# Kernel optimization log

Measured on AMD Instinct MI355X. Metric: run time of the kernel, lower is better.

The kernel has to match this reference:

```python
import jax, jax.numpy as jnp
import numpy as np

P, N, NF = 4, 871, 512            # num_meta_paths, node_size (hardcoded 871 in source), node_feature_size
XDIM = 116 * 116                   # x_proj input dim, hardcoded Linear(116*116, nf)
BETA, LAMBDA_WL, GAMMA = 0.1, 0.1, 0.1


def _xavier(k, shape):
    fan_in, fan_out = shape[0], shape[-1]
    bound = np.sqrt(6.0 / (fan_in + fan_out))
    return jax.random.uniform(k, shape, jnp.float32, -bound, bound)


def setup_inputs() -> dict:
    key = jax.random.key(0)
    ks = jax.random.split(key, 12)
    return {
        "z_stack": jax.random.normal(ks[0], (P, N, NF), jnp.float32),
        "x_orig": jax.random.normal(ks[1], (1, 116, 116), jnp.float32),
        "W": _xavier(ks[2], (N, 1)),
        "b": jax.random.uniform(ks[3], (N, 1), jnp.float32),
        "q": _xavier(ks[4], (N, NF)),
        "xp_w": _xavier(ks[5], (XDIM, NF)),
        "xp_b": jnp.zeros((NF,), jnp.float32),
        "w1": _xavier(ks[6], (2 * NF, 512)), "b1": jnp.zeros((512,), jnp.float32),
        "w2": _xavier(ks[7], (512, 256)), "b2": jnp.zeros((256,), jnp.float32),
        "w3": _xavier(ks[8], (256, 1)), "b3": jnp.zeros((1,), jnp.float32),
        "perm": jax.random.permutation(ks[9], N).astype(jnp.int32),
    }


def _mi_mlp(t, w1, b1, w2, b2, w3, b3):
    h = jax.nn.relu(t @ w1 + b1)
    h = jax.nn.relu(h @ w2 + b2)
    return h @ w3 + b3  # [N, 1]


def reference(z_stack, x_orig, W, b, q, xp_w, xp_b, w1, b1, w2, b2, w3, b3, perm):
    # --- vectorized form of the per-node loop:
    # score_p = mean_i( tanh(W_i * z[p,i,:] + b_i) . q_i )
    zt = jnp.tanh(W[None] * z_stack + b[None])            # [P,N,NF]
    scores = jnp.mean(jnp.sum(zt * q[None], axis=-1), axis=-1)  # [P]
    proportions = scores / jnp.sum(scores)
    attn = jax.nn.softmax(proportions)                    # [P] (no isomorphic pairs -> no overwrite)
    # layer_out_p = attn_p * z_p + z_p ; emb = sum_p layer_out_p
    emb = jnp.einsum('p,pnf->nf', 1.0 + attn, z_stack)    # [N,NF]
    # --- estimate_MI(x_orig, emb, mi_estimator_xz)
    x = jnp.broadcast_to(x_orig.reshape(1, -1), (N, XDIM))
    xh = x @ xp_w + xp_b                                  # [N,NF]
    t0 = jnp.concatenate([xh, emb], axis=1)               # [N,2NF]
    t1 = jnp.concatenate([xh, emb[perm]], axis=1)
    mi_lb = jnp.mean(_mi_mlp(t0, w1, b1, w2, b2, w3, b3)) - jnp.log(
        jnp.mean(jnp.exp(_mi_mlp(t1, w1, b1, w2, b2, w3, b3))) + 1e-8)
    I_XZ = jnp.clip(mi_lb, 0.0)
    # y_labels=None -> I_ZY = 0 ; empty isomorphic_pairs -> wl_loss = 0
    total_loss = I_XZ - BETA * 0.0 + LAMBDA_WL * 0.0 + GAMMA * jnp.sum(attn)
    return emb, total_loss
```

## Files before the change

### kernel.cpp

```cpp
#include <hip/hip_runtime.h>
#include <hip/hip_bf16.h>
#include <math.h>

#define NMETA  4
#define NNODE  871
#define NFEAT  512
#define XDIM   (116*116)
#define ZPLANE (NNODE*NFEAT)
#define MT     55

#define NXB    175
#define XROWS  77

#define WS_SPART  16
#define WS_C1P    256
#define WS_XHP    8448
#define WS_V      98304
#define WS_W1P    99328
#define WS_W2P    230400
#define WS_FXHP   263168
#define WS_FPACK  263344
#define WS_FC1    263368
#define WS_FSP    263376
#define WS_FV     263436
#define MAGICF    0x13579BDFu

typedef short v8s __attribute__((ext_vector_type(8)));
typedef float v4f __attribute__((ext_vector_type(4)));

static __device__ __forceinline__ short f2bf(float f) {
  __hip_bfloat16 h = __float2bfloat16(f);
  return *reinterpret_cast<short*>(&h);
}

static __device__ __forceinline__ unsigned ldflag(const float* ws, int off) {
  return __hip_atomic_load((const unsigned*)&ws[off], __ATOMIC_RELAXED,
                           __HIP_MEMORY_SCOPE_AGENT);
}
static __device__ __forceinline__ void stflag(float* ws, int off) {
  __builtin_amdgcn_fence(__ATOMIC_RELEASE, "agent");
  __hip_atomic_store((unsigned*)&ws[off], MAGICF, __ATOMIC_RELAXED,
                     __HIP_MEMORY_SCOPE_AGENT);
}

__global__ __launch_bounds__(1024) void k_all(const float* __restrict__ z,
                                              const float* __restrict__ x,
                                              const float* __restrict__ W,
                                              const float* __restrict__ b,
                                              const float* __restrict__ q,
                                              const float* __restrict__ xpw,
                                              const float* __restrict__ xpb,
                                              const float* __restrict__ w1,
                                              const float* __restrict__ b1,
                                              const float* __restrict__ w2,
                                              const float* __restrict__ b2,
                                              const float* __restrict__ w3,
                                              const float* __restrict__ b3,
                                              float* __restrict__ ws,
                                              float* __restrict__ out,
                                              short* __restrict__ w1p,
                                              short* __restrict__ w2p) {
  __shared__ __align__(16) char pool[37376];
  const int blk = blockIdx.x;
  const int tid = threadIdx.x;

  if (blk < MT) {
    short* embs = (short*)pool;
    short* h2a  = (short*)(pool + 16384);
    float* cs   = (float*)(pool + 32768);
    float* spl  = (float*)(pool + 34816);
    float* sred = (float*)(pool + 35712);
    float* cf   = (float*)(pool + 35968);
    float* vred = (float*)(pool + 36000);
    float* wred = (float*)(pool + 37088);

    const int r0 = blk * 16;
    const int oc = tid & 63;
    const int row = tid >> 6;
    const int gr = r0 + row;
    const bool valid = gr < NNODE;

    const float4* z4 = (const float4*)z;
    const float4* q4 = (const float4*)q;
    float4 za0, za1, zb0, zb1, zc0, zc1, zd0, zd1, qa, qb;
    float wi = 0.f, bi = 0.f;
    const int zi = gr * 128 + oc * 2;
    if (valid) {
      za0 = z4[zi];                 za1 = z4[zi + 1];
      zb0 = z4[NNODE*128 + zi];     zb1 = z4[NNODE*128 + zi + 1];
      zc0 = z4[2*NNODE*128 + zi];   zc1 = z4[2*NNODE*128 + zi + 1];
      zd0 = z4[3*NNODE*128 + zi];   zd1 = z4[3*NNODE*128 + zi + 1];
      qa  = q4[gr * 128 + oc * 2];  qb  = q4[gr * 128 + oc * 2 + 1];
      wi = W[gr]; bi = b[gr];
    } else {
      za0 = za1 = zb0 = zb1 = zc0 = zc1 = zd0 = zd1 = (float4){0,0,0,0};
      qa = qb = (float4){0,0,0,0};
    }

    auto dot8 = [&](const float4& u0, const float4& u1) -> float {
      return tanhf(wi*u0.x + bi)*qa.x + tanhf(wi*u0.y + bi)*qa.y
           + tanhf(wi*u0.z + bi)*qa.z + tanhf(wi*u0.w + bi)*qa.w
           + tanhf(wi*u1.x + bi)*qb.x + tanhf(wi*u1.y + bi)*qb.y
           + tanhf(wi*u1.z + bi)*qb.z + tanhf(wi*u1.w + bi)*qb.w;
    };
    float sp0 = valid ? dot8(za0, za1) : 0.f;
    float sp1 = valid ? dot8(zb0, zb1) : 0.f;
    float sp2 = valid ? dot8(zc0, zc1) : 0.f;
    float sp3 = valid ? dot8(zd0, zd1) : 0.f;
#pragma unroll
    for (int m = 1; m < 64; m <<= 1) {
      sp0 += __shfl_xor(sp0, m); sp1 += __shfl_xor(sp1, m);
      sp2 += __shfl_xor(sp2, m); sp3 += __shfl_xor(sp3, m);
    }
    if (oc == 0) {
      sred[row*4+0] = sp0; sred[row*4+1] = sp1;
      sred[row*4+2] = sp2; sred[row*4+3] = sp3;
    }
    __syncthreads();
    if (tid < 4) {
      float s = 0.f;
#pragma unroll
      for (int r = 0; r < 16; ++r) s += sred[r*4 + tid];
      ws[WS_SPART + tid * 55 + blk] = s;
    }
    __syncthreads();
    if (tid == 0) stflag(ws, WS_FSP + blk);

    for (;;) {
      int ok = 1;
      if (tid < 55) ok = (ldflag(ws, WS_FSP + tid) == MAGICF);
      if (__syncthreads_and(ok)) break;
      __builtin_amdgcn_s_sleep(2);
    }
    __builtin_amdgcn_fence(__ATOMIC_ACQUIRE, "agent");
    if (tid < 220) spl[tid] = ws[WS_SPART + tid];
    __syncthreads();
    if (tid == 0) {
      float sv[NMETA], sum = 0.f;
#pragma unroll
      for (int p = 0; p < NMETA; ++p) {
        float s = 0.f;
        for (int c = 0; c < MT; ++c) s += spl[p * 55 + c];
        sv[p] = s / (float)NNODE;
        sum += sv[p];
      }
      float m = -1e30f;
#pragma unroll
      for (int p = 0; p < NMETA; ++p) { sv[p] = sv[p] / sum; m = fmaxf(m, sv[p]); }
      float es = 0.f;
#pragma unroll
      for (int p = 0; p < NMETA; ++p) { sv[p] = expf(sv[p] - m); es += sv[p]; }
#pragma unroll
      for (int p = 0; p < NMETA; ++p) cf[p] = 1.f + sv[p] / es;
    }
    __syncthreads();
    const float c0 = cf[0], c1c = cf[1], c2 = cf[2], c3 = cf[3];

    {
      const int slot = oc * 16 + (row ^ (oc & 15));
      v8s h;
      if (valid) {
        float4 r0v, r1v;
        r0v.x = c0*za0.x + c1c*zb0.x + c2*zc0.x + c3*zd0.x;
        r0v.y = c0*za0.y + c1c*zb0.y + c2*zc0.y + c3*zd0.y;
        r0v.z = c0*za0.z + c1c*zb0.z + c2*zc0.z + c3*zd0.z;
        r0v.w = c0*za0.w + c1c*zb0.w + c2*zc0.w + c3*zd0.w;
        r1v.x = c0*za1.x + c1c*zb1.x + c2*zc1.x + c3*zd1.x;
        r1v.y = c0*za1.y + c1c*zb1.y + c2*zc1.y + c3*zd1.y;
        r1v.z = c0*za1.z + c1c*zb1.z + c2*zc1.z + c3*zd1.z;
        r1v.w = c0*za1.w + c1c*zb1.w + c2*zc1.w + c3*zd1.w;
        ((float4*)out)[zi] = r0v;
        ((float4*)out)[zi + 1] = r1v;
        h[0] = f2bf(r0v.x); h[1] = f2bf(r0v.y); h[2] = f2bf(r0v.z); h[3] = f2bf(r0v.w);
        h[4] = f2bf(r1v.x); h[5] = f2bf(r1v.y); h[6] = f2bf(r1v.z); h[7] = f2bf(r1v.w);
      } else {
        h = (v8s){0,0,0,0,0,0,0,0};
      }
      *(v8s*)(embs + slot * 8) = h;
    }
    __syncthreads();

    for (;;) {
      int ok = 1;
      if (tid < 16) ok = (ldflag(ws, WS_FPACK + tid) == MAGICF);
      else if (tid < 20) ok = (ldflag(ws, WS_FC1 + (tid - 16)) == MAGICF);
      if (__syncthreads_and(ok)) break;
      __builtin_amdgcn_s_sleep(2);
    }
    __builtin_amdgcn_fence(__ATOMIC_ACQUIRE, "agent");
    if (tid < 512) {
      float a = 0.f;
#pragma unroll
      for (int k = 0; k < 4; ++k) a += ws[WS_C1P + k * 512 + tid];
      cs[tid] = a;
    }
    __syncthreads();

    const int lane = tid & 63, w = tid >> 6;
    const int n15 = lane & 15, quad = lane >> 4;
    v4f e[2];
#pragma unroll
    for (int ct = 0; ct < 2; ++ct) e[ct] = (v4f){0.f, 0.f, 0.f, 0.f};
#pragma unroll
    for (int kb = 0; kb < 16; ++kb) {
      const int koct = kb * 4 + quad;
      v8s a = *(const v8s*)(embs + (koct * 16 + (n15 ^ (koct & 15))) * 8);
      const short* B = w1p + kb * 16384 + w * 1024 + quad * 128 + n15 * 8;
#pragma unroll
      for (int ct = 0; ct < 2; ++ct) {
        v8s bb = *(const v8s*)(B + ct * 512);
        e[ct] = __builtin_amdgcn_mfma_f32_16x16x32_bf16(a, bb, e[ct], 0, 0, 0);
      }
    }
#pragma unroll
    for (int ct = 0; ct < 2; ++ct) {
      const int col = w * 32 + ct * 16 + n15;
      const int koct = col >> 3, j = col & 7;
#pragma unroll
      for (int r = 0; r < 4; ++r) {
        const int m = quad * 4 + r;
        h2a[(koct * 16 + (m ^ (koct & 15))) * 8 + j] = f2bf(fmaxf(e[ct][r] + cs[col], 0.f));
      }
    }
    __syncthreads();

    for (;;) {
      int ok = 1;
      if (tid < 4) ok = (ldflag(ws, WS_FPACK + 16 + tid) == MAGICF);
      if (__syncthreads_and(ok)) break;
      __builtin_amdgcn_s_sleep(2);
    }
    __builtin_amdgcn_fence(__ATOMIC_ACQUIRE, "agent");

    v4f g = (v4f){0.f, 0.f, 0.f, 0.f};
#pragma unroll
    for (int kb = 0; kb < 16; ++kb) {
      const int koct = kb * 4 + quad;
      v8s a = *(const v8s*)(h2a + (koct * 16 + (n15 ^ (koct & 15))) * 8);
      v8s bb = *(const v8s*)(w2p + kb * 8192 + w * 512 + quad * 128 + n15 * 8);
      g = __builtin_amdgcn_mfma_f32_16x16x32_bf16(a, bb, g, 0, 0, 0);
    }
    {
      const int col = w * 16 + n15;
      const float b2v = b2[col], w3v = w3[col];
#pragma unroll
      for (int r = 0; r < 4; ++r) {
        float s = fmaxf(g[r] + b2v, 0.f) * w3v;
        s += __shfl_xor(s, 1);
        s += __shfl_xor(s, 2);
        s += __shfl_xor(s, 4);
        s += __shfl_xor(s, 8);
        if (n15 == 0) vred[(quad * 4 + r) * 17 + w] = s;
      }
    }
    __syncthreads();
    if (tid < 16) {
      float acc = 0.f;
#pragma unroll
      for (int ww = 0; ww < 16; ++ww) acc += vred[tid * 17 + ww];
      const int grow = r0 + tid;
      if (grow < NNODE) ws[WS_V + grow] = acc;
    }
    __syncthreads();
    if (tid == 0) stflag(ws, WS_FV + blk);

    if (blk == 0) {
      for (;;) {
        int ok = 1;
        if (tid < 55) ok = (ldflag(ws, WS_FV + tid) == MAGICF);
        if (__syncthreads_and(ok)) break;
        __builtin_amdgcn_s_sleep(2);
      }
      __builtin_amdgcn_fence(__ATOMIC_ACQUIRE, "agent");
      const float bias = b3[0];
      float s0 = 0.f, s1 = 0.f;
      if (tid < NNODE) {
        float xv = ws[WS_V + tid] + bias;
        s0 = xv; s1 = expf(xv);
      }
#pragma unroll
      for (int m = 1; m < 64; m <<= 1) { s0 += __shfl_xor(s0, m); s1 += __shfl_xor(s1, m); }
      if (lane == 0) { wred[w * 2] = s0; wred[w * 2 + 1] = s1; }
      __syncthreads();
      if (tid == 0) {
        float t0 = 0.f, t1 = 0.f;
#pragma unroll
        for (int ww = 0; ww < 16; ++ww) { t0 += wred[ww * 2]; t1 += wred[ww * 2 + 1]; }
        float m0 = t0 / (float)NNODE;
        float m1 = t1 / (float)NNODE;
        float mi = m0 - logf(m1 + 1e-8f);
        out[ZPLANE] = fmaxf(mi, 0.f) + 0.1f;
      }
    }
  } else if (blk < MT + NXB) {
    const int xb = blk - MT;
    const int d0 = xb * XROWS;
    const int rows = min(XROWS, XDIM - d0);
    float* xs = (float*)pool;
    float4* redx = (float4*)(pool + 320);
    if (tid < rows) xs[tid] = x[d0 + tid];
    __syncthreads();
    const int f4 = tid & 127;
    const int rp = tid >> 7;
    float4 acc = {0.f, 0.f, 0.f, 0.f};
    const float4* xp4 = (const float4*)xpw;
    for (int r = rp; r < rows; r += 8) {
      const float xv = xs[r];
      const float4 wv = xp4[(size_t)(d0 + r) * 128 + f4];
      acc.x += xv * wv.x; acc.y += xv * wv.y; acc.z += xv * wv.z; acc.w += xv * wv.w;
    }
    if (rp) redx[(rp - 1) * 128 + f4] = acc;
    __syncthreads();
    if (!rp) {
#pragma unroll
      for (int g = 0; g < 7; ++g) {
        float4 t = redx[g * 128 + f4];
        acc.x += t.x; acc.y += t.y; acc.z += t.z; acc.w += t.w;
      }
      ((float4*)(ws + WS_XHP + (size_t)xb * 512))[f4] = acc;
    }
    __syncthreads();
    if (tid == 0) stflag(ws, WS_FXHP + xb);
  } else if (blk < MT + NXB + 4) {
    const int bk = blk - (MT + NXB);
    float* xh = (float*)pool;
    float* redr = (float*)(pool + 512);
    float4* redg = (float4*)(pool + 4608);
    for (;;) {
      int ok = 1;
      if (tid < NXB) ok = (ldflag(ws, WS_FXHP + tid) == MAGICF);
      if (__syncthreads_and(ok)) break;
      __builtin_amdgcn_s_sleep(2);
    }
    __builtin_amdgcn_fence(__ATOMIC_ACQUIRE, "agent");
    const int f = tid & 127;
    const int part = tid >> 7;
    {
      float s = 0.f;
      for (int p = part; p < NXB; p += 8) s += ws[WS_XHP + (size_t)p * 512 + bk * 128 + f];
      redr[tid] = s;
    }
    __syncthreads();
    if (tid < 128) {
      float t = xpb[bk * 128 + tid];
#pragma unroll
      for (int g = 0; g < 8; ++g) t += redr[g * 128 + tid];
      xh[tid] = t;
    }
    __syncthreads();
    const int j4 = tid & 127;
    const int fg = tid >> 7;
    float4 acc = {0.f, 0.f, 0.f, 0.f};
    const float4* w14 = (const float4*)w1;
#pragma unroll
    for (int ff = 0; ff < 16; ++ff) {
      const int fr = bk * 128 + fg * 16 + ff;
      const float xv = xh[fg * 16 + ff];
      const float4 wv = w14[(size_t)fr * 128 + j4];
      acc.x += xv * wv.x; acc.y += xv * wv.y; acc.z += xv * wv.z; acc.w += xv * wv.w;
    }
    if (fg) redg[(fg - 1) * 128 + j4] = acc;
    __syncthreads();
    if (!fg) {
#pragma unroll
      for (int g = 0; g < 7; ++g) {
        float4 t = redg[g * 128 + j4];
        acc.x += t.x; acc.y += t.y; acc.z += t.z; acc.w += t.w;
      }
      if (bk == 0) {
        acc.x += b1[j4 * 4 + 0]; acc.y += b1[j4 * 4 + 1];
        acc.z += b1[j4 * 4 + 2]; acc.w += b1[j4 * 4 + 3];
      }
      ((float4*)(ws + WS_C1P + (size_t)bk * 512))[j4] = acc;
    }
    __syncthreads();
    if (tid == 0) stflag(ws, WS_FC1 + bk);
  } else {
    const int pb = blk - (MT + NXB + 4);
    if (pb < 16) {
      const int s0 = pb * 16384;
#pragma unroll
      for (int it = 0; it < 16; ++it) {
        const int s = s0 + it * 1024 + tid;
        const int k = s >> 9, n = s & 511;
        const int t = (k >> 5) * 16384 + (n >> 4) * 512 + ((k >> 3) & 3) * 128
                    + (n & 15) * 8 + (k & 7);
        w1p[t] = f2bf(w1[(size_t)(512 + k) * 512 + n]);
      }
    } else {
      const int o0 = (pb - 16) * 16384;
#pragma unroll
      for (int it = 0; it < 16; ++it) {
        const int o = o0 + it * 1024 + tid;
        const int k = o >> 8, n = o & 255;
        const int t = (k >> 5) * 8192 + (n >> 4) * 512 + ((k >> 3) & 3) * 128
                    + (n & 15) * 8 + (k & 7);
        w2p[t] = f2bf(w2[(size_t)k * 256 + n]);
      }
    }
    __syncthreads();
    if (tid == 0) stflag(ws, WS_FPACK + pb);
  }
}

extern "C" void kernel_launch(void* const* d_in, const int* in_sizes, int n_in,
                              void* d_out, int out_size, void* d_ws, size_t ws_size,
                              hipStream_t stream) {
  const float* z   = (const float*)d_in[0];
  const float* x   = (const float*)d_in[1];
  const float* W   = (const float*)d_in[2];
  const float* b   = (const float*)d_in[3];
  const float* q   = (const float*)d_in[4];
  const float* xpw = (const float*)d_in[5];
  const float* xpb = (const float*)d_in[6];
  const float* w1  = (const float*)d_in[7];
  const float* b1  = (const float*)d_in[8];
  const float* w2  = (const float*)d_in[9];
  const float* b2  = (const float*)d_in[10];
  const float* w3  = (const float*)d_in[11];
  const float* b3  = (const float*)d_in[12];
  float* out = (float*)d_out;
  float* ws  = (float*)d_ws;

  short* w1p = (short*)(ws + WS_W1P);
  short* w2p = (short*)(ws + WS_W2P);

  k_all<<<MT + NXB + 4 + 20, 1024, 0, stream>>>(z, x, W, b, q, xpw, xpb, w1, b1,
                                                w2, b2, w3, b3, ws, out, w1p, w2p);
}
```

Baseline: 152.1 us.

## Split persistent kernel into front and fused kernels, replacing spin-wait flags

Splits the single flag-synchronized kernel into two launches. The first launch computes the x-projection partials, the score partials, the weight packing and the first-layer constant. The second launch computes emb and runs both MLP layers, then finishes with a last-block atomic-counter reduction for the MI term. Most inter-block spin-waits are replaced by the kernel boundary, and the x-projection is spread over more blocks with fewer rows each. The cost is one extra launch. The z tile is also read twice (once per kernel), and the c1 blocks still spin on x-projection flags inside the first kernel.

Measured after the change: 143.8 us. 1.06x faster.

```diff
diff --git a/kernel.cpp b/kernel.cpp
--- a/kernel.cpp
+++ b/kernel.cpp
@@ -9,20 +9,17 @@
 #define ZPLANE (NNODE*NFEAT)
 #define MT     55
 
-#define NXB    175
-#define XROWS  77
-
+#define NXB    254
+#define XROWS  53
+
+#define WS_CNT    12
 #define WS_SPART  16
 #define WS_C1P    256
-#define WS_XHP    8448
-#define WS_V      98304
-#define WS_W1P    99328
-#define WS_W2P    230400
-#define WS_FXHP   263168
-#define WS_FPACK  263344
-#define WS_FC1    263368
-#define WS_FSP    263376
-#define WS_FV     263436
+#define WS_XHP    2560
+#define WS_V      132608
+#define WS_W1P    133504
+#define WS_W2P    264576
+#define WS_FXHP   297344
 #define MAGICF    0x13579BDFu
 
 typedef short v8s __attribute__((ext_vector_type(8)));
@@ -43,60 +40,71 @@
                      __HIP_MEMORY_SCOPE_AGENT);
 }
 
-__global__ __launch_bounds__(1024) void k_all(const float* __restrict__ z,
-                                              const float* __restrict__ x,
-                                              const float* __restrict__ W,
-                                              const float* __restrict__ b,
-                                              const float* __restrict__ q,
-                                              const float* __restrict__ xpw,
-                                              const float* __restrict__ xpb,
-                                              const float* __restrict__ w1,
-                                              const float* __restrict__ b1,
-                                              const float* __restrict__ w2,
-                                              const float* __restrict__ b2,
-                                              const float* __restrict__ w3,
-                                              const float* __restrict__ b3,
-                                              float* __restrict__ ws,
-                                              float* __restrict__ out,
-                                              short* __restrict__ w1p,
-                                              short* __restrict__ w2p) {
-  __shared__ __align__(16) char pool[37376];
+__global__ __launch_bounds__(1024) void k_front(const float* __restrict__ x,
+                                                const float* __restrict__ xpw,
+                                                const float* __restrict__ w1,
+                                                const float* __restrict__ w2,
+                                                const float* __restrict__ z,
+                                                const float* __restrict__ W,
+                                                const float* __restrict__ b,
+                                                const float* __restrict__ q,
+                                                const float* __restrict__ xpb,
+                                                const float* __restrict__ b1,
+                                                float* __restrict__ ws,
+                                                short* __restrict__ w1p,
+                                                short* __restrict__ w2p) {
   const int blk = blockIdx.x;
   const int tid = threadIdx.x;
 
-  if (blk < MT) {
-    short* embs = (short*)pool;
-    short* h2a  = (short*)(pool + 16384);
-    float* cs   = (float*)(pool + 32768);
-    float* spl  = (float*)(pool + 34816);
-    float* sred = (float*)(pool + 35712);
-    float* cf   = (float*)(pool + 35968);
-    float* vred = (float*)(pool + 36000);
-    float* wred = (float*)(pool + 37088);
-
-    const int r0 = blk * 16;
+  if (blk < NXB) {
+    const int d0 = blk * XROWS;
+    const int rows = min(XROWS, XDIM - d0);
+    __shared__ float xs[XROWS];
+    __shared__ float4 redx[7][128];
+    if (tid < rows) xs[tid] = x[d0 + tid];
+    __syncthreads();
+    const int f4 = tid & 127;
+    const int g = tid >> 7;
+    float4 acc = {0.f, 0.f, 0.f, 0.f};
+    const float4* xp4 = (const float4*)xpw;
+    for (int r = g; r < rows; r += 8) {
+      const float xv = xs[r];
+      const float4 wv = xp4[(size_t)(d0 + r) * 128 + f4];
+      acc.x += xv * wv.x; acc.y += xv * wv.y; acc.z += xv * wv.z; acc.w += xv * wv.w;
+    }
+    if (g) redx[g - 1][f4] = acc;
+    __syncthreads();
+    if (!g) {
+#pragma unroll
+      for (int k = 0; k < 7; ++k) {
+        float4 t = redx[k][f4];
+        acc.x += t.x; acc.y += t.y; acc.z += t.z; acc.w += t.w;
+      }
+      ((float4*)(ws + WS_XHP + (size_t)blk * 512))[f4] = acc;
+    }
+    __syncthreads();
+    if (tid == 0) stflag(ws, WS_FXHP + blk);
+  } else if (blk < NXB + MT) {
+    const int sb = blk - NXB;
+    const int row = tid >> 6;
     const int oc = tid & 63;
-    const int row = tid >> 6;
-    const int gr = r0 + row;
+    const int gr = sb * 16 + row;
     const bool valid = gr < NNODE;
-
     const float4* z4 = (const float4*)z;
     const float4* q4 = (const float4*)q;
     float4 za0, za1, zb0, zb1, zc0, zc1, zd0, zd1, qa, qb;
     float wi = 0.f, bi = 0.f;
+    za0 = za1 = zb0 = zb1 = zc0 = zc1 = zd0 = zd1 = (float4){0,0,0,0};
+    qa = qb = (float4){0,0,0,0};
     const int zi = gr * 128 + oc * 2;
     if (valid) {
       za0 = z4[zi];                 za1 = z4[zi + 1];
       zb0 = z4[NNODE*128 + zi];     zb1 = z4[NNODE*128 + zi + 1];
       zc0 = z4[2*NNODE*128 + zi];   zc1 = z4[2*NNODE*128 + zi + 1];
       zd0 = z4[3*NNODE*128 + zi];   zd1 = z4[3*NNODE*128 + zi + 1];
-      qa  = q4[gr * 128 + oc * 2];  qb  = q4[gr * 128 + oc * 2 + 1];
+      qa  = q4[zi];                 qb  = q4[zi + 1];
       wi = W[gr]; bi = b[gr];
-    } else {
-      za0 = za1 = zb0 = zb1 = zc0 = zc1 = zd0 = zd1 = (float4){0,0,0,0};
-      qa = qb = (float4){0,0,0,0};
-    }
-
+    }
     auto dot8 = [&](const float4& u0, const float4& u1) -> float {
       return tanhf(wi*u0.x + bi)*qa.x + tanhf(wi*u0.y + bi)*qa.y
            + tanhf(wi*u0.z + bi)*qa.z + tanhf(wi*u0.w + bi)*qa.w
@@ -112,271 +120,20 @@
       sp0 += __shfl_xor(sp0, m); sp1 += __shfl_xor(sp1, m);
       sp2 += __shfl_xor(sp2, m); sp3 += __shfl_xor(sp3, m);
     }
+    __shared__ float sred[16][4];
     if (oc == 0) {
-      sred[row*4+0] = sp0; sred[row*4+1] = sp1;
-      sred[row*4+2] = sp2; sred[row*4+3] = sp3;
+      sred[row][0] = sp0; sred[row][1] = sp1;
+      sred[row][2] = sp2; sred[row][3] = sp3;
     }
     __syncthreads();
     if (tid < 4) {
       float s = 0.f;
 #pragma unroll
-      for (int r = 0; r < 16; ++r) s += sred[r*4 + tid];
-      ws[WS_SPART + tid * 55 + blk] = s;
-    }
-    __syncthreads();
-    if (tid == 0) stflag(ws, WS_FSP + blk);
-
-    for (;;) {
-      int ok = 1;
-      if (tid < 55) ok = (ldflag(ws, WS_FSP + tid) == MAGICF);
-      if (__syncthreads_and(ok)) break;
-      __builtin_amdgcn_s_sleep(2);
-    }
-    __builtin_amdgcn_fence(__ATOMIC_ACQUIRE, "agent");
-    if (tid < 220) spl[tid] = ws[WS_SPART + tid];
-    __syncthreads();
-    if (tid == 0) {
-      float sv[NMETA], sum = 0.f;
-#pragma unroll
-      for (int p = 0; p < NMETA; ++p) {
-        float s = 0.f;
-        for (int c = 0; c < MT; ++c) s += spl[p * 55 + c];
-        sv[p] = s / (float)NNODE;
-        sum += sv[p];
-      }
-      float m = -1e30f;
-#pragma unroll
-      for (int p = 0; p < NMETA; ++p) { sv[p] = sv[p] / sum; m = fmaxf(m, sv[p]); }
-      float es = 0.f;
-#pragma unroll
-      for (int p = 0; p < NMETA; ++p) { sv[p] = expf(sv[p] - m); es += sv[p]; }
-#pragma unroll
-      for (int p = 0; p < NMETA; ++p) cf[p] = 1.f + sv[p] / es;
-    }
-    __syncthreads();
-    const float c0 = cf[0], c1c = cf[1], c2 = cf[2], c3 = cf[3];
-
-    {
-      const int slot = oc * 16 + (row ^ (oc & 15));
-      v8s h;
-      if (valid) {
-        float4 r0v, r1v;
-        r0v.x = c0*za0.x + c1c*zb0.x + c2*zc0.x + c3*zd0.x;
-        r0v.y = c0*za0.y + c1c*zb0.y + c2*zc0.y + c3*zd0.y;
-        r0v.z = c0*za0.z + c1c*zb0.z + c2*zc0.z + c3*zd0.z;
-        r0v.w = c0*za0.w + c1c*zb0.w + c2*zc0.w + c3*zd0.w;
-        r1v.x = c0*za1.x + c1c*zb1.x + c2*zc1.x + c3*zd1.x;
-        r1v.y = c0*za1.y + c1c*zb1.y + c2*zc1.y + c3*zd1.y;
-        r1v.z = c0*za1.z + c1c*zb1.z + c2*zc1.z + c3*zd1.z;
-        r1v.w = c0*za1.w + c1c*zb1.w + c2*zc1.w + c3*zd1.w;
-        ((float4*)out)[zi] = r0v;
-        ((float4*)out)[zi + 1] = r1v;
-        h[0] = f2bf(r0v.x); h[1] = f2bf(r0v.y); h[2] = f2bf(r0v.z); h[3] = f2bf(r0v.w);
-        h[4] = f2bf(r1v.x); h[5] = f2bf(r1v.y); h[6] = f2bf(r1v.z); h[7] = f2bf(r1v.w);
-      } else {
-        h = (v8s){0,0,0,0,0,0,0,0};
-      }
-      *(v8s*)(embs + slot * 8) = h;
-    }
-    __syncthreads();
-
-    for (;;) {
-      int ok = 1;
-      if (tid < 16) ok = (ldflag(ws, WS_FPACK + tid) == MAGICF);
-      else if (tid < 20) ok = (ldflag(ws, WS_FC1 + (tid - 16)) == MAGICF);
-      if (__syncthreads_and(ok)) break;
-      __builtin_amdgcn_s_sleep(2);
-    }
-    __builtin_amdgcn_fence(__ATOMIC_ACQUIRE, "agent");
-    if (tid < 512) {
-      float a = 0.f;
-#pragma unroll
-      for (int k = 0; k < 4; ++k) a += ws[WS_C1P + k * 512 + tid];
-      cs[tid] = a;
-    }
-    __syncthreads();
-
-    const int lane = tid & 63, w = tid >> 6;
-    const int n15 = lane & 15, quad = lane >> 4;
-    v4f e[2];
-#pragma unroll
-    for (int ct = 0; ct < 2; ++ct) e[ct] = (v4f){0.f, 0.f, 0.f, 0.f};
-#pragma unroll
-    for (int kb = 0; kb < 16; ++kb) {
-      const int koct = kb * 4 + quad;
-      v8s a = *(const v8s*)(embs + (koct * 16 + (n15 ^ (koct & 15))) * 8);
-      const short* B = w1p + kb * 16384 + w * 1024 + quad * 128 + n15 * 8;
-#pragma unroll
-      for (int ct = 0; ct < 2; ++ct) {
-        v8s bb = *(const v8s*)(B + ct * 512);
-        e[ct] = __builtin_amdgcn_mfma_f32_16x16x32_bf16(a, bb, e[ct], 0, 0, 0);
-      }
-    }
-#pragma unroll
-    for (int ct = 0; ct < 2; ++ct) {
-      const int col = w * 32 + ct * 16 + n15;
-      const int koct = col >> 3, j = col & 7;
-#pragma unroll
-      for (int r = 0; r < 4; ++r) {
-        const int m = quad * 4 + r;
-        h2a[(koct * 16 + (m ^ (koct & 15))) * 8 + j] = f2bf(fmaxf(e[ct][r] + cs[col], 0.f));
-      }
-    }
-    __syncthreads();
-
-    for (;;) {
-      int ok = 1;
-      if (tid < 4) ok = (ldflag(ws, WS_FPACK + 16 + tid) == MAGICF);
-      if (__syncthreads_and(ok)) break;
-      __builtin_amdgcn_s_sleep(2);
-    }
-    __builtin_amdgcn_fence(__ATOMIC_ACQUIRE, "agent");
-
-    v4f g = (v4f){0.f, 0.f, 0.f, 0.f};
-#pragma unroll
-    for (int kb = 0; kb < 16; ++kb) {
-      const int koct = kb * 4 + quad;
-      v8s a = *(const v8s*)(h2a + (koct * 16 + (n15 ^ (koct & 15))) * 8);
-      v8s bb = *(const v8s*)(w2p + kb * 8192 + w * 512 + quad * 128 + n15 * 8);
-      g = __builtin_amdgcn_mfma_f32_16x16x32_bf16(a, bb, g, 0, 0, 0);
-    }
-    {
-      const int col = w * 16 + n15;
-      const float b2v = b2[col], w3v = w3[col];
-#pragma unroll
-      for (int r = 0; r < 4; ++r) {
-        float s = fmaxf(g[r] + b2v, 0.f) * w3v;
-        s += __shfl_xor(s, 1);
-        s += __shfl_xor(s, 2);
-        s += __shfl_xor(s, 4);
-        s += __shfl_xor(s, 8);
-        if (n15 == 0) vred[(quad * 4 + r) * 17 + w] = s;
-      }
-    }
-    __syncthreads();
-    if (tid < 16) {
-      float acc = 0.f;
-#pragma unroll
-      for (int ww = 0; ww < 16; ++ww) acc += vred[tid * 17 + ww];
-      const int grow = r0 + tid;
-      if (grow < NNODE) ws[WS_V + grow] = acc;
-    }
-    __syncthreads();
-    if (tid == 0) stflag(ws, WS_FV + blk);
-
-    if (blk == 0) {
-      for (;;) {
-        int ok = 1;
-        if (tid < 55) ok = (ldflag(ws, WS_FV + tid) == MAGICF);
-        if (__syncthreads_and(ok)) break;
-        __builtin_amdgcn_s_sleep(2);
-      }
-      __builtin_amdgcn_fence(__ATOMIC_ACQUIRE, "agent");
-      const float bias = b3[0];
-      float s0 = 0.f, s1 = 0.f;
-      if (tid < NNODE) {
-        float xv = ws[WS_V + tid] + bias;
-        s0 = xv; s1 = expf(xv);
-      }
-#pragma unroll
-      for (int m = 1; m < 64; m <<= 1) { s0 += __shfl_xor(s0, m); s1 += __shfl_xor(s1, m); }
-      if (lane == 0) { wred[w * 2] = s0; wred[w * 2 + 1] = s1; }
-      __syncthreads();
-      if (tid == 0) {
-        float t0 = 0.f, t1 = 0.f;
-#pragma unroll
-        for (int ww = 0; ww < 16; ++ww) { t0 += wred[ww * 2]; t1 += wred[ww * 2 + 1]; }
-        float m0 = t0 / (float)NNODE;
-        float m1 = t1 / (float)NNODE;
-        float mi = m0 - logf(m1 + 1e-8f);
-        out[ZPLANE] = fmaxf(mi, 0.f) + 0.1f;
-      }
-    }
-  } else if (blk < MT + NXB) {
-    const int xb = blk - MT;
-    const int d0 = xb * XROWS;
-    const int rows = min(XROWS, XDIM - d0);
-    float* xs = (float*)pool;
-    float4* redx = (float4*)(pool + 320);
-    if (tid < rows) xs[tid] = x[d0 + tid];
-    __syncthreads();
-    const int f4 = tid & 127;
-    const int rp = tid >> 7;
-    float4 acc = {0.f, 0.f, 0.f, 0.f};
-    const float4* xp4 = (const float4*)xpw;
-    for (int r = rp; r < rows; r += 8) {
-      const float xv = xs[r];
-      const float4 wv = xp4[(size_t)(d0 + r) * 128 + f4];
-      acc.x += xv * wv.x; acc.y += xv * wv.y; acc.z += xv * wv.z; acc.w += xv * wv.w;
-    }
-    if (rp) redx[(rp - 1) * 128 + f4] = acc;
-    __syncthreads();
-    if (!rp) {
-#pragma unroll
-      for (int g = 0; g < 7; ++g) {
-        float4 t = redx[g * 128 + f4];
-        acc.x += t.x; acc.y += t.y; acc.z += t.z; acc.w += t.w;
-      }
-      ((float4*)(ws + WS_XHP + (size_t)xb * 512))[f4] = acc;
-    }
-    __syncthreads();
-    if (tid == 0) stflag(ws, WS_FXHP + xb);
-  } else if (blk < MT + NXB + 4) {
-    const int bk = blk - (MT + NXB);
-    float* xh = (float*)pool;
-    float* redr = (float*)(pool + 512);
-    float4* redg = (float4*)(pool + 4608);
-    for (;;) {
-      int ok = 1;
-      if (tid < NXB) ok = (ldflag(ws, WS_FXHP + tid) == MAGICF);
-      if (__syncthreads_and(ok)) break;
-      __builtin_amdgcn_s_sleep(2);
-    }
-    __builtin_amdgcn_fence(__ATOMIC_ACQUIRE, "agent");
-    const int f = tid & 127;
-    const int part = tid >> 7;
-    {
-      float s = 0.f;
-      for (int p = part; p < NXB; p += 8) s += ws[WS_XHP + (size_t)p * 512 + bk * 128 + f];
-      redr[tid] = s;
-    }
-    __syncthreads();
-    if (tid < 128) {
-      float t = xpb[bk * 128 + tid];
-#pragma unroll
-      for (int g = 0; g < 8; ++g) t += redr[g * 128 + tid];
-      xh[tid] = t;
-    }
-    __syncthreads();
-    const int j4 = tid & 127;
-    const int fg = tid >> 7;
-    float4 acc = {0.f, 0.f, 0.f, 0.f};
-    const float4* w14 = (const float4*)w1;
-#pragma unroll
-    for (int ff = 0; ff < 16; ++ff) {
-      const int fr = bk * 128 + fg * 16 + ff;
-      const float xv = xh[fg * 16 + ff];
-      const float4 wv = w14[(size_t)fr * 128 + j4];
-      acc.x += xv * wv.x; acc.y += xv * wv.y; acc.z += xv * wv.z; acc.w += xv * wv.w;
-    }
-    if (fg) redg[(fg - 1) * 128 + j4] = acc;
-    __syncthreads();
-    if (!fg) {
-#pragma unroll
-      for (int g = 0; g < 7; ++g) {
-        float4 t = redg[g * 128 + j4];
-        acc.x += t.x; acc.y += t.y; acc.z += t.z; acc.w += t.w;
-      }
-      if (bk == 0) {
-        acc.x += b1[j4 * 4 + 0]; acc.y += b1[j4 * 4 + 1];
-        acc.z += b1[j4 * 4 + 2]; acc.w += b1[j4 * 4 + 3];
-      }
-      ((float4*)(ws + WS_C1P + (size_t)bk * 512))[j4] = acc;
-    }
-    __syncthreads();
-    if (tid == 0) stflag(ws, WS_FC1 + bk);
-  } else {
-    const int pb = blk - (MT + NXB + 4);
+      for (int r = 0; r < 16; ++r) s += sred[r][tid];
+      ws[WS_SPART + tid * 55 + sb] = s;
+    }
+  } else if (blk < NXB + MT + 20) {
+    const int pb = blk - (NXB + MT);
     if (pb < 16) {
       const int s0 = pb * 16384;
 #pragma unroll
@@ -398,8 +155,240 @@
         w2p[t] = f2bf(w2[(size_t)k * 256 + n]);
       }
     }
-    __syncthreads();
-    if (tid == 0) stflag(ws, WS_FPACK + pb);
+  } else {
+    const int bk = blk - (NXB + MT + 20);
+    __shared__ float xh[128];
+    __shared__ float redr[1024];
+    __shared__ float4 redg[7][128];
+    if (tid == 1023) *(unsigned*)&ws[WS_CNT] = 0u;
+    for (;;) {
+      int ok = 1;
+      if (tid < NXB) ok = (ldflag(ws, WS_FXHP + tid) == MAGICF);
+      if (__syncthreads_and(ok)) break;
+      __builtin_amdgcn_s_sleep(2);
+    }
+    __builtin_amdgcn_fence(__ATOMIC_ACQUIRE, "agent");
+    const int f = tid & 127;
+    const int part = tid >> 7;
+    {
+      float s = 0.f;
+      for (int p = part; p < NXB; p += 8)
+        s += ws[WS_XHP + (size_t)p * 512 + bk * 128 + f];
+      redr[tid] = s;
+    }
+    __syncthreads();
+    if (tid < 128) {
+      float t = xpb[bk * 128 + tid];
+#pragma unroll
+      for (int g = 0; g < 8; ++g) t += redr[g * 128 + tid];
+      xh[tid] = t;
+    }
+    __syncthreads();
+    const int j4 = tid & 127;
+    const int fg = tid >> 7;
+    float4 acc = {0.f, 0.f, 0.f, 0.f};
+    const float4* w14 = (const float4*)w1;
+#pragma unroll
+    for (int ff = 0; ff < 16; ++ff) {
+      const int fr = bk * 128 + fg * 16 + ff;
+      const float xv = xh[fg * 16 + ff];
+      const float4 wv = w14[(size_t)fr * 128 + j4];
+      acc.x += xv * wv.x; acc.y += xv * wv.y; acc.z += xv * wv.z; acc.w += xv * wv.w;
+    }
+    if (fg) redg[fg - 1][j4] = acc;
+    __syncthreads();
+    if (!fg) {
+#pragma unroll
+      for (int g = 0; g < 7; ++g) {
+        float4 t = redg[g][j4];
+        acc.x += t.x; acc.y += t.y; acc.z += t.z; acc.w += t.w;
+      }
+      if (bk == 0) {
+        acc.x += b1[j4 * 4 + 0]; acc.y += b1[j4 * 4 + 1];
+        acc.z += b1[j4 * 4 + 2]; acc.w += b1[j4 * 4 + 3];
+      }
+      ((float4*)(ws + WS_C1P + (size_t)bk * 512))[j4] = acc;
+    }
+  }
+}
+
+__global__ __launch_bounds__(1024) void k_fused(const float* __restrict__ z,
+                                                float* __restrict__ ws,
+                                                float* __restrict__ out,
+                                                const short* __restrict__ w1p,
+                                                const short* __restrict__ w2p,
+                                                const float* __restrict__ b2,
+                                                const float* __restrict__ w3,
+                                                const float* __restrict__ b3) {
+  __shared__ __align__(16) short embs[8192];
+  __shared__ __align__(16) short h2a[8192];
+  __shared__ float cs[512];
+  __shared__ float rf0[1024], rf1[1024];
+  __shared__ float vred[16][17];
+  __shared__ float cf[4];
+  __shared__ float svred[4];
+  const int tid = threadIdx.x;
+  const int r0 = blockIdx.x * 16;
+  const int oc = tid & 63;
+  const int row = tid >> 6;
+  const int gr = r0 + row;
+  const bool valid = gr < NNODE;
+
+  const float4* z4 = (const float4*)z;
+  float4 za0, za1, zb0, zb1, zc0, zc1, zd0, zd1;
+  za0 = za1 = zb0 = zb1 = zc0 = zc1 = zd0 = zd1 = (float4){0,0,0,0};
+  const int zi = gr * 128 + oc * 2;
+  if (valid) {
+    za0 = z4[zi];                 za1 = z4[zi + 1];
+    zb0 = z4[NNODE*128 + zi];     zb1 = z4[NNODE*128 + zi + 1];
+    zc0 = z4[2*NNODE*128 + zi];   zc1 = z4[2*NNODE*128 + zi + 1];
+    zd0 = z4[3*NNODE*128 + zi];   zd1 = z4[3*NNODE*128 + zi + 1];
+  }
+
+  if (tid < 512) {
+    float a = 0.f;
+#pragma unroll
+    for (int k = 0; k < 4; ++k) a += ws[WS_C1P + k * 512 + tid];
+    cs[tid] = a;
+  }
+
+  {
+    const int w4 = tid >> 6;
+    if (w4 < 4) {
+      float v = (oc < 55) ? ws[WS_SPART + w4 * 55 + oc] : 0.f;
+#pragma unroll
+      for (int m = 1; m < 64; m <<= 1) v += __shfl_xor(v, m);
+      if (oc == 0) svred[w4] = v;
+    }
+  }
+  __syncthreads();
+  if (tid == 0) {
+    float sv[NMETA], sum = 0.f;
+#pragma unroll
+    for (int p = 0; p < NMETA; ++p) { sv[p] = svred[p] / (float)NNODE; sum += sv[p]; }
+    float m = -1e30f;
+#pragma unroll
+    for (int p = 0; p < NMETA; ++p) { sv[p] = sv[p] / sum; m = fmaxf(m, sv[p]); }
+    float es = 0.f;
+#pragma unroll
+    for (int p = 0; p < NMETA; ++p) { sv[p] = expf(sv[p] - m); es += sv[p]; }
+#pragma unroll
+    for (int p = 0; p < NMETA; ++p) cf[p] = 1.f + sv[p] / es;
+  }
+  __syncthreads();
+  const float c0 = cf[0], c1c = cf[1], c2 = cf[2], c3 = cf[3];
+
+  {
+    const int slot = oc * 16 + (row ^ (oc & 15));
+    v8s h;
+    if (valid) {
+      float4 r0v, r1v;
+      r0v.x = c0*za0.x + c1c*zb0.x + c2*zc0.x + c3*zd0.x;
+      r0v.y = c0*za0.y + c1c*zb0.y + c2*zc0.y + c3*zd0.y;
+      r0v.z = c0*za0.z + c1c*zb0.z + c2*zc0.z + c3*zd0.z;
+      r0v.w = c0*za0.w + c1c*zb0.w + c2*zc0.w + c3*zd0.w;
+      r1v.x = c0*za1.x + c1c*zb1.x + c2*zc1.x + c3*zd1.x;
+      r1v.y = c0*za1.y + c1c*zb1.y + c2*zc1.y + c3*zd1.y;
+      r1v.z = c0*za1.z + c1c*zb1.z + c2*zc1.z + c3*zd1.z;
+      r1v.w = c0*za1.w + c1c*zb1.w + c2*zc1.w + c3*zd1.w;
+      ((float4*)out)[zi] = r0v;
+      ((float4*)out)[zi + 1] = r1v;
+      h[0] = f2bf(r0v.x); h[1] = f2bf(r0v.y); h[2] = f2bf(r0v.z); h[3] = f2bf(r0v.w);
+      h[4] = f2bf(r1v.x); h[5] = f2bf(r1v.y); h[6] = f2bf(r1v.z); h[7] = f2bf(r1v.w);
+    } else {
+      h = (v8s){0,0,0,0,0,0,0,0};
+    }
+    *(v8s*)(embs + slot * 8) = h;
+  }
+  __syncthreads();
+
+  const int lane = tid & 63, w = tid >> 6;
+  const int n15 = lane & 15, quad = lane >> 4;
+  v4f e[2];
+#pragma unroll
+  for (int ct = 0; ct < 2; ++ct) e[ct] = (v4f){0.f, 0.f, 0.f, 0.f};
+#pragma unroll
+  for (int kb = 0; kb < 16; ++kb) {
+    const int koct = kb * 4 + quad;
+    v8s a = *(const v8s*)(embs + (koct * 16 + (n15 ^ (koct & 15))) * 8);
+    const short* B = w1p + kb * 16384 + w * 1024 + quad * 128 + n15 * 8;
+#pragma unroll
+    for (int ct = 0; ct < 2; ++ct) {
+      v8s bb = *(const v8s*)(B + ct * 512);
+      e[ct] = __builtin_amdgcn_mfma_f32_16x16x32_bf16(a, bb, e[ct], 0, 0, 0);
+    }
+  }
+#pragma unroll
+  for (int ct = 0; ct < 2; ++ct) {
+    const int col = w * 32 + ct * 16 + n15;
+    const int koct = col >> 3, j = col & 7;
+#pragma unroll
+    for (int r = 0; r < 4; ++r) {
+      const int m = quad * 4 + r;
+      h2a[(koct * 16 + (m ^ (koct & 15))) * 8 + j] = f2bf(fmaxf(e[ct][r] + cs[col], 0.f));
+    }
+  }
+  __syncthreads();
+
+  v4f g = (v4f){0.f, 0.f, 0.f, 0.f};
+#pragma unroll
+  for (int kb = 0; kb < 16; ++kb) {
+    const int koct = kb * 4 + quad;
+    v8s a = *(const v8s*)(h2a + (koct * 16 + (n15 ^ (koct & 15))) * 8);
+    v8s bb = *(const v8s*)(w2p + kb * 8192 + w * 512 + quad * 128 + n15 * 8);
+    g = __builtin_amdgcn_mfma_f32_16x16x32_bf16(a, bb, g, 0, 0, 0);
+  }
+  {
+    const int col = w * 16 + n15;
+    const float b2v = b2[col], w3v = w3[col];
+#pragma unroll
+    for (int r = 0; r < 4; ++r) {
+      float s = fmaxf(g[r] + b2v, 0.f) * w3v;
+      s += __shfl_xor(s, 1);
+      s += __shfl_xor(s, 2);
+      s += __shfl_xor(s, 4);
+      s += __shfl_xor(s, 8);
+      if (n15 == 0) vred[quad * 4 + r][w] = s;
+    }
+  }
+  __syncthreads();
+  if (tid < 16) {
+    float acc = 0.f;
+#pragma unroll
+    for (int ww = 0; ww < 16; ++ww) acc += vred[tid][ww];
+    const int grow = r0 + tid;
+    if (grow < NNODE) ws[WS_V + grow] = acc;
+  }
+
+  __shared__ unsigned last;
+  __syncthreads();
+  if (tid == 0) {
+    __threadfence();
+    unsigned old = atomicAdd((unsigned int*)&ws[WS_CNT], 1u);
+    last = (old == MT - 1) ? 1u : 0u;
+  }
+  __syncthreads();
+  if (last) {
+    __builtin_amdgcn_fence(__ATOMIC_ACQUIRE, "agent");
+    const float bias = b3[0];
+    float s0 = 0.f, s1 = 0.f;
+    for (int i = tid; i < NNODE; i += 1024) {
+      float xv = ws[WS_V + i] + bias;
+      s0 += xv;
+      s1 += expf(xv);
+    }
+    rf0[tid] = s0; rf1[tid] = s1;
+    __syncthreads();
+    for (int s = 512; s > 0; s >>= 1) {
+      if (tid < s) { rf0[tid] += rf0[tid + s]; rf1[tid] += rf1[tid + s]; }
+      __syncthreads();
+    }
+    if (tid == 0) {
+      float m0 = rf0[0] / (float)NNODE;
+      float m1 = rf1[0] / (float)NNODE;
+      float mi = m0 - logf(m1 + 1e-8f);
+      out[ZPLANE] = fmaxf(mi, 0.f) + 0.1f;
+    }
   }
 }
 
@@ -425,6 +414,7 @@
   short* w1p = (short*)(ws + WS_W1P);
   short* w2p = (short*)(ws + WS_W2P);
 
-  k_all<<<MT + NXB + 4 + 20, 1024, 0, stream>>>(z, x, W, b, q, xpw, xpb, w1, b1,
-                                                w2, b2, w3, b3, ws, out, w1p, w2p);
-}
+  k_front<<<NXB + MT + 20 + 4, 1024, 0, stream>>>(x, xpw, w1, w2, z, W, b, q,
+                                                  xpb, b1, ws, w1p, w2p);
+  k_fused<<<MT, 1024, 0, stream>>>(z, ws, out, w1p, w2p, b2, w3, b3);
+}
```
